# Kernel tuning notes

Measured on AMD Instinct MI355X. Metric: run time of the kernel, lower is better.

Reference implementation:

```python
import jax, jax.numpy as jnp
import numpy as np

MOL_SIZE = 64      # points per molecule (all molecules equal-size -> block-diagonal attn)
NUM_HEADS = 8
CUTOFF = 8.0
NUM_RBF = 32
LN_EPS = 1e-5


def setup_inputs() -> dict:
    key = jax.random.key(0)
    ks = jax.random.split(key, 6)
    B, K, hidden = 1024, MOL_SIZE, 512
    H = NUM_HEADS
    N = B * K
    h = jax.random.normal(ks[0], (N, hidden), jnp.float32)
    pos = jax.random.normal(ks[1], (N, 3), jnp.float32) * 3.0  # spread so dists hit RBF centers
    batch = jnp.repeat(jnp.arange(B, dtype=jnp.int32), K)
    s = lambda fin: 1.0 / np.sqrt(fin)
    centers = jnp.linspace(0.0, CUTOFF, NUM_RBF).astype(jnp.float32)  # RBFEncoder buffer
    w_rbf = jax.random.normal(ks[2], (NUM_RBF, H), jnp.float32) * s(NUM_RBF)
    b_rbf = jnp.zeros((H,), jnp.float32)
    w_qkv = jax.random.normal(ks[3], (hidden, 3 * hidden), jnp.float32) * s(hidden)
    b_qkv = jnp.zeros((3 * hidden,), jnp.float32)
    w_out = jax.random.normal(ks[4], (hidden, hidden), jnp.float32) * s(hidden)
    b_out = jnp.zeros((hidden,), jnp.float32)
    gamma = jnp.ones((hidden,), jnp.float32)
    beta = jnp.zeros((hidden,), jnp.float32)
    return {"h": h, "pos": pos, "batch": batch, "centers": centers,
            "w_rbf": w_rbf, "b_rbf": b_rbf, "w_qkv": w_qkv, "b_qkv": b_qkv,
            "w_out": w_out, "b_out": b_out, "gamma": gamma, "beta": beta}


def reference(h, pos, batch, centers, w_rbf, b_rbf, w_qkv, b_qkv, w_out, b_out, gamma, beta):
    N, hidden = h.shape
    K = MOL_SIZE
    B = N // K
    H = NUM_HEADS
    D = hidden // H
    width = (CUTOFF / NUM_RBF) ** 2
    scale = D ** -0.5

    # equal-size contiguous molecules -> reshape equals per-molecule loop
    hb = h.reshape(B, K, hidden)
    pb = pos.reshape(B, K, 3)

    qkv = hb @ w_qkv + b_qkv                      # [B,K,3*hidden]
    q, k, v = jnp.split(qkv, 3, axis=-1)
    q = q.reshape(B, K, H, D)
    k = k.reshape(B, K, H, D)
    v = v.reshape(B, K, H, D)

    diff = pb[:, :, None, :] - pb[:, None, :, :]  # [B,K,K,3]
    dist = jnp.sqrt(jnp.maximum(jnp.sum(diff * diff, axis=-1), 1e-12))  # torch.cdist
    rbf = jnp.exp(-((dist[..., None] - centers) ** 2) / width)          # [B,K,K,R]
    bias = jnp.transpose(rbf @ w_rbf + b_rbf, (0, 3, 1, 2))             # [B,H,K,K]

    attn = jnp.einsum('bkhd,bjhd->bhkj', q, k) * scale + bias
    attn = jax.nn.softmax(attn, axis=-1)
    agg = jnp.einsum('bhkj,bjhd->bkhd', attn, v).reshape(B, K, hidden)
    out = agg @ w_out + b_out

    y = hb + out
    mu = jnp.mean(y, axis=-1, keepdims=True)
    var = jnp.var(y, axis=-1, keepdims=True)
    y = (y - mu) / jnp.sqrt(var + LN_EPS) * gamma + beta
    return y.reshape(N, hidden)
```

## Files before the change

### kernel.cpp

```cpp
#include <hip/hip_runtime.h>
#include <hip/hip_bf16.h>


#define HID 512
#define TBL 1024
#define DMAX 12.0f

typedef __attribute__((ext_vector_type(4))) float f32x4;
typedef __attribute__((ext_vector_type(8))) short bhalf8;

__device__ __forceinline__ short f2bf(float f) {
    union { float f; unsigned u; } x; x.f = f;
    unsigned u = x.u;
    unsigned r = (u + 0x7FFFu + ((u >> 16) & 1u)) >> 16;
    return (short)r;
}

__device__ __forceinline__ void gld_lds16(const void* g, void* l) {
    __builtin_amdgcn_global_load_lds((const __attribute__((address_space(1))) void*)g,
                                     (__attribute__((address_space(3))) void*)l, 16, 0, 0);
}

__global__ __launch_bounds__(256) void k_prep_w(const float* __restrict__ w_qkv,
                                                const float* __restrict__ w_out,
                                                short* __restrict__ wqT,
                                                short* __restrict__ woT) {
    __shared__ short tile[64][68];
    const int t = threadIdx.x;
    int bt = blockIdx.x;
    const float* src; short* dst; int sld, tk, tc, swz;
    if (bt < 192) { src = w_qkv; dst = wqT; sld = 1536; tk = bt & 7; tc = bt >> 3; swz = 1; }
    else { int b2 = bt - 192; src = w_out; dst = woT; sld = 512; tk = b2 & 7; tc = b2 >> 3; swz = 0; }
#pragma unroll
    for (int p = 0; p < 4; ++p) {
        int s = t + 256 * p;
        int r = s >> 4, sg = s & 15;
        const float4 v = *(const float4*)(src + (tk * 64 + r) * sld + tc * 64 + sg * 4);
        tile[r][sg * 4 + 0] = f2bf(v.x);
        tile[r][sg * 4 + 1] = f2bf(v.y);
        tile[r][sg * 4 + 2] = f2bf(v.z);
        tile[r][sg * 4 + 3] = f2bf(v.w);
    }
    __syncthreads();
#pragma unroll
    for (int p = 0; p < 16; ++p) {
        int o = t + 256 * p;
        int c = o >> 6, k = o & 63;
        int kk = swz ? (k ^ ((c & 7) << 3)) : k;
        dst[(tc * 64 + c) * 512 + tk * 64 + kk] = tile[k][c];
    }
}

__global__ __launch_bounds__(256) void k_prep_tbl(const float* __restrict__ centers,
                                                  const float* __restrict__ w_rbf,
                                                  const float* __restrict__ b_rbf,
                                                  float* __restrict__ tbl) {
    int idx = blockIdx.x * 256 + threadIdx.x;
    int hh = idx >> 10, i = idx & (TBL - 1);
    float d = (float)i * (DMAX / (float)(TBL - 1));
    float s = b_rbf[hh];
    const float invw = 1.0f / 0.0625f;
#pragma unroll 4
    for (int r = 0; r < 32; ++r) {
        float tt = d - centers[r];
        s += w_rbf[r * 8 + hh] * expf(-(tt * tt) * invw);
    }
    tbl[idx] = s;
}

__global__ __launch_bounds__(256) void k_prep_h(const float* __restrict__ h,
                                                short* __restrict__ hbf,
                                                int molbase) {
    size_t i = ((size_t)blockIdx.x * 256 + threadIdx.x) * 8;
    const float* src = h + (size_t)molbase * 64 * HID + i;
    float4 a = *(const float4*)src;
    float4 b = *(const float4*)(src + 4);
    short s8[8];
    s8[0] = f2bf(a.x); s8[1] = f2bf(a.y); s8[2] = f2bf(a.z); s8[3] = f2bf(a.w);
    s8[4] = f2bf(b.x); s8[5] = f2bf(b.y); s8[6] = f2bf(b.z); s8[7] = f2bf(b.w);
    int row = (int)(i >> 9);
    size_t o = i ^ (size_t)((row & 7) << 3);
    *(int4*)(hbf + o) = *(int4*)s8;
}

__global__ __launch_bounds__(512) void k_qkv(const short* __restrict__ hbf,
                                             const float* __restrict__ b_qkv,
                                             const short* __restrict__ wqT,
                                             short* __restrict__ qkvb) {
    __shared__ __align__(16) short As[128 * 64];
    __shared__ __align__(16) short Bs[256 * 64];
    const int t = threadIdx.x;
    const int lane = t & 63, wave = t >> 6;
    const int l16 = lane & 15, g = lane >> 4;
    const int wrow = wave >> 2, wcol = wave & 3;

    int wg = blockIdx.x;
    wg = (wg & 7) * 192 + (wg >> 3);
    const int bx = wg & 255, by = wg >> 8;
    const int R0l = bx * 128;
    const int C0 = by * 256;

    f32x4 acc[4][4];
#pragma unroll
    for (int i = 0; i < 4; ++i)
#pragma unroll
        for (int j = 0; j < 4; ++j) acc[i][j] = (f32x4){0.f, 0.f, 0.f, 0.f};

    const int lrow = lane >> 3, lslot = lane & 7;
    const int axor = (l16 & 7) << 3;

    for (int kc = 0; kc < 8; ++kc) {
        const int kb = kc * 64;
#pragma unroll
        for (int j = 0; j < 2; ++j) {
            int row = wave * 16 + j * 8 + lrow;
            gld_lds16(hbf + (size_t)(R0l + row) * HID + kb + lslot * 8,
                      (char*)As + wave * 2048 + j * 1024 + lane * 16);
        }
#pragma unroll
        for (int j = 0; j < 4; ++j) {
            int row = wave * 32 + j * 8 + lrow;
            gld_lds16(wqT + (size_t)(C0 + row) * HID + kb + lslot * 8,
                      (char*)Bs + wave * 4096 + j * 1024 + lane * 16);
        }
        __syncthreads();
#pragma unroll
        for (int kk = 0; kk < 2; ++kk) {
            const int c8 = kk * 32 + g * 8;
            const int cs = c8 ^ axor;
            bhalf8 af[4], bf[4];
#pragma unroll
            for (int mt = 0; mt < 4; ++mt)
                af[mt] = *(const bhalf8*)(&As[(wrow * 64 + mt * 16 + l16) * 64 + cs]);
#pragma unroll
            for (int nt = 0; nt < 4; ++nt)
                bf[nt] = *(const bhalf8*)(&Bs[(wcol * 64 + nt * 16 + l16) * 64 + cs]);
#pragma unroll
            for (int mt = 0; mt < 4; ++mt)
#pragma unroll
                for (int nt = 0; nt < 4; ++nt)
                    acc[mt][nt] = __builtin_amdgcn_mfma_f32_16x16x32_bf16(
                        af[mt], bf[nt], acc[mt][nt], 0, 0, 0);
        }
        __syncthreads();
    }

    const int sec = C0 >> 9;
    const float mul = (sec == 0) ? 0.125f : 1.0f;
#pragma unroll
    for (int nt = 0; nt < 4; ++nt) {
        int c = C0 + wcol * 64 + nt * 16 + l16;
        float bv = b_qkv[c];
        int head = (c >> 6) & 7, d = c & 63;
#pragma unroll
        for (int mt = 0; mt < 4; ++mt) {
            int rowl = R0l + wrow * 64 + mt * 16 + g * 4;
            int mol_local = rowl >> 6;
            int rloc = rowl & 63;
            short* panel = qkvb + (size_t)((mol_local * 3 + sec) * 8 + head) * 4096;
            if (sec == 2) {
                short4 s4;
                s4.x = f2bf(acc[mt][nt][0] + bv);
                s4.y = f2bf(acc[mt][nt][1] + bv);
                s4.z = f2bf(acc[mt][nt][2] + bv);
                s4.w = f2bf(acc[mt][nt][3] + bv);
                *(short4*)(panel + d * 64 + rloc) = s4;
            } else {
#pragma unroll
                for (int r = 0; r < 4; ++r)
                    panel[(rloc + r) * 64 + d] = f2bf((acc[mt][nt][r] + bv) * mul);
            }
        }
    }
}

__global__ __launch_bounds__(512) void k_fused(const short* __restrict__ qkvb,
                                               const float* __restrict__ pos,
                                               const float* __restrict__ tbl,
                                               const float* __restrict__ h,
                                               const short* __restrict__ woT,
                                               const float* __restrict__ b_out,
                                               const float* __restrict__ gamma,
                                               const float* __restrict__ beta,
                                               float* __restrict__ out,
                                               int molbase) {
    __shared__ __align__(16) short uP[8 * 4096];
    __shared__ float s_tbl[8 * 1032];
    __shared__ float s_px[64], s_py[64], s_pz[64];
    __shared__ float red[64 * 16];
    __shared__ float mr[64 * 2];

    const int t = threadIdx.x;
    const int wave = t >> 6, lane = t & 63;
    const int l16 = lane & 15, g = lane >> 4;
    const int mol_local = blockIdx.x;
    const int rowbase = (molbase + mol_local) * 64;

    for (int i = t; i < 8 * TBL; i += 512)
        s_tbl[(i >> 10) * 1032 + (i & (TBL - 1))] = tbl[i];
    if (t < 64) {
        s_px[t] = pos[(rowbase + t) * 3 + 0];
        s_py[t] = pos[(rowbase + t) * 3 + 1];
        s_pz[t] = pos[(rowbase + t) * 3 + 2];
    }
    __syncthreads();

    const short* qp = qkvb + ((size_t)(mol_local * 3 + 0) * 8 + wave) * 4096;
    const short* kp = qkvb + ((size_t)(mol_local * 3 + 1) * 8 + wave) * 4096;
    const short* vt = qkvb + ((size_t)(mol_local * 3 + 2) * 8 + wave) * 4096;

    f32x4 sacc[4][4];
#pragma unroll
    for (int i = 0; i < 4; ++i)
#pragma unroll
        for (int j = 0; j < 4; ++j) sacc[i][j] = (f32x4){0.f, 0.f, 0.f, 0.f};
#pragma unroll
    for (int kk = 0; kk < 2; ++kk) {
        bhalf8 qa[4], kb[4];
#pragma unroll
        for (int mt = 0; mt < 4; ++mt)
            qa[mt] = *(const bhalf8*)(qp + (mt * 16 + l16) * 64 + kk * 32 + g * 8);
#pragma unroll
        for (int nt = 0; nt < 4; ++nt)
            kb[nt] = *(const bhalf8*)(kp + (nt * 16 + l16) * 64 + kk * 32 + g * 8);
#pragma unroll
        for (int mt = 0; mt < 4; ++mt)
#pragma unroll
            for (int nt = 0; nt < 4; ++nt)
                sacc[mt][nt] = __builtin_amdgcn_mfma_f32_16x16x32_bf16(
                    qa[mt], kb[nt], sacc[mt][nt], 0, 0, 0);
    }

    const float tscale = (float)(TBL - 1) / DMAX;
    const float* T = s_tbl + wave * 1032;
#pragma unroll
    for (int nt = 0; nt < 4; ++nt) {
        int col = nt * 16 + l16;
        float cx = s_px[col], cy = s_py[col], cz = s_pz[col];
#pragma unroll
        for (int mt = 0; mt < 4; ++mt) {
#pragma unroll
            for (int r = 0; r < 4; ++r) {
                int row = mt * 16 + g * 4 + r;
                float dx = s_px[row] - cx, dy = s_py[row] - cy, dz = s_pz[row] - cz;
                float dd = fmaf(dx, dx, fmaf(dy, dy, dz * dz));
                float dist = sqrtf(fmaxf(dd, 1e-12f));
                float u = fminf(dist, DMAX) * tscale;
                int i = (int)u; if (i > TBL - 2) i = TBL - 2;
                float fr = u - (float)i;
                float t0 = T[i];
                sacc[mt][nt][r] += fmaf(fr, T[i + 1] - t0, t0);
            }
        }
    }

    float inv[4][4];
    short* Pw = uP + wave * 4096;
#pragma unroll
    for (int mt = 0; mt < 4; ++mt) {
#pragma unroll
        for (int r = 0; r < 4; ++r) {
            float m = fmaxf(fmaxf(sacc[mt][0][r], sacc[mt][1][r]),
                            fmaxf(sacc[mt][2][r], sacc[mt][3][r]));
#pragma unroll
            for (int off = 1; off < 16; off <<= 1) m = fmaxf(m, __shfl_xor(m, off, 64));
            float e[4], ssum = 0.f;
#pragma unroll
            for (int nt = 0; nt < 4; ++nt) { e[nt] = __expf(sacc[mt][nt][r] - m); ssum += e[nt]; }
#pragma unroll
            for (int off = 1; off < 16; off <<= 1) ssum += __shfl_xor(ssum, off, 64);
            inv[mt][r] = 1.0f / ssum;
            int row = mt * 16 + g * 4 + r;
            int rho = row & 7;
#pragma unroll
            for (int nt = 0; nt < 4; ++nt) {
                int c = nt * 16 + l16;
                Pw[row * 64 + (((c >> 3) ^ rho) << 3) + (c & 7)] = f2bf(e[nt]);
            }
        }
    }

    f32x4 oacc[4][4];
#pragma unroll
    for (int i = 0; i < 4; ++i)
#pragma unroll
        for (int j = 0; j < 4; ++j) oacc[i][j] = (f32x4){0.f, 0.f, 0.f, 0.f};
#pragma unroll
    for (int kk = 0; kk < 2; ++kk) {
        bhalf8 pa[4], vb[4];
#pragma unroll
        for (int mt = 0; mt < 4; ++mt)
            pa[mt] = *(const bhalf8*)(Pw + (mt * 16 + l16) * 64 +
                                      (((kk * 4 + g) ^ (l16 & 7)) << 3));
#pragma unroll
        for (int nt = 0; nt < 4; ++nt)
            vb[nt] = *(const bhalf8*)(vt + (nt * 16 + l16) * 64 + kk * 32 + g * 8);
#pragma unroll
        for (int mt = 0; mt < 4; ++mt)
#pragma unroll
            for (int nt = 0; nt < 4; ++nt)
                oacc[mt][nt] = __builtin_amdgcn_mfma_f32_16x16x32_bf16(
                    pa[mt], vb[nt], oacc[mt][nt], 0, 0, 0);
    }
#pragma unroll
    for (int mt = 0; mt < 4; ++mt)
#pragma unroll
        for (int nt = 0; nt < 4; ++nt)
#pragma unroll
            for (int r = 0; r < 4; ++r) oacc[mt][nt][r] *= inv[mt][r];

    __syncthreads();

#pragma unroll
    for (int mt = 0; mt < 4; ++mt) {
#pragma unroll
        for (int r = 0; r < 4; ++r) {
            int row = mt * 16 + g * 4 + r;
            int rho = row & 7;
#pragma unroll
            for (int nt = 0; nt < 4; ++nt) {
                int c = wave * 64 + nt * 16 + l16;
                uP[row * 512 + (((c >> 3) ^ rho) << 3) + (c & 7)] = f2bf(oacc[mt][nt][r]);
            }
        }
    }
    __syncthreads();

    f32x4 pacc[4][4];
#pragma unroll
    for (int i = 0; i < 4; ++i)
#pragma unroll
        for (int j = 0; j < 4; ++j) pacc[i][j] = (f32x4){0.f, 0.f, 0.f, 0.f};
#pragma unroll 4
    for (int kc = 0; kc < 16; ++kc) {
        bhalf8 af[4], bw[4];
#pragma unroll
        for (int mt = 0; mt < 4; ++mt)
            af[mt] = *(const bhalf8*)(uP + (mt * 16 + l16) * 512 +
                                      (((kc * 4 + g) ^ (l16 & 7)) << 3));
#pragma unroll
        for (int nt = 0; nt < 4; ++nt)
            bw[nt] = *(const bhalf8*)(woT + (size_t)(wave * 64 + nt * 16 + l16) * HID +
                                      kc * 32 + g * 8);
#pragma unroll
        for (int mt = 0; mt < 4; ++mt)
#pragma unroll
            for (int nt = 0; nt < 4; ++nt)
                pacc[mt][nt] = __builtin_amdgcn_mfma_f32_16x16x32_bf16(
                    af[mt], bw[nt], pacc[mt][nt], 0, 0, 0);
    }

#pragma unroll
    for (int mt = 0; mt < 4; ++mt) {
#pragma unroll
        for (int r = 0; r < 4; ++r) {
            int row = mt * 16 + g * 4 + r;
            float rs = 0.f, rq = 0.f;
#pragma unroll
            for (int nt = 0; nt < 4; ++nt) {
                int col = wave * 64 + nt * 16 + l16;
                float v = pacc[mt][nt][r] + b_out[col] +
                          h[(size_t)(rowbase + row) * HID + col];
                pacc[mt][nt][r] = v;
                rs += v;
                rq = fmaf(v, v, rq);
            }
#pragma unroll
            for (int off = 1; off < 16; off <<= 1) {
                rs += __shfl_xor(rs, off, 64);
                rq += __shfl_xor(rq, off, 64);
            }
            if (l16 == 0) {
                red[row * 16 + wave * 2 + 0] = rs;
                red[row * 16 + wave * 2 + 1] = rq;
            }
        }
    }
    __syncthreads();
    if (t < 64) {
        float s = 0.f, q = 0.f;
#pragma unroll
        for (int w = 0; w < 8; ++w) {
            s += red[t * 16 + w * 2 + 0];
            q += red[t * 16 + w * 2 + 1];
        }
        float mean = s * (1.0f / 512.0f);
        float var = q * (1.0f / 512.0f) - mean * mean;
        mr[t * 2 + 0] = mean;
        mr[t * 2 + 1] = rsqrtf(var + 1e-5f);
    }
    __syncthreads();
#pragma unroll
    for (int mt = 0; mt < 4; ++mt) {
#pragma unroll
        for (int r = 0; r < 4; ++r) {
            int row = mt * 16 + g * 4 + r;
            float mean = mr[row * 2 + 0], rstd = mr[row * 2 + 1];
#pragma unroll
            for (int nt = 0; nt < 4; ++nt) {
                int col = wave * 64 + nt * 16 + l16;
                out[(size_t)(rowbase + row) * HID + col] =
                    fmaf((pacc[mt][nt][r] - mean) * rstd, gamma[col], beta[col]);
            }
        }
    }
}

extern "C" void kernel_launch(void* const* d_in, const int* in_sizes, int n_in,
                              void* d_out, int out_size, void* d_ws, size_t ws_size,
                              hipStream_t stream) {
    (void)in_sizes; (void)n_in; (void)out_size; (void)ws_size;
    const float* h       = (const float*)d_in[0];
    const float* pos     = (const float*)d_in[1];
    const float* centers = (const float*)d_in[3];
    const float* w_rbf   = (const float*)d_in[4];
    const float* b_rbf   = (const float*)d_in[5];
    const float* w_qkv   = (const float*)d_in[6];
    const float* b_qkv   = (const float*)d_in[7];
    const float* w_out   = (const float*)d_in[8];
    const float* b_out   = (const float*)d_in[9];
    const float* gamma   = (const float*)d_in[10];
    const float* beta    = (const float*)d_in[11];
    float* out = (float*)d_out;

    char* ws = (char*)d_ws;
    short* wqT  = (short*)ws;
    short* woT  = (short*)(ws + 1572864);
    float* tbl  = (float*)(ws + 2097152);
    short* hbf  = (short*)(ws + 2162688);
    short* qkvb = (short*)(ws + 35717120);

    k_prep_w<<<256, 256, 0, stream>>>(w_qkv, w_out, wqT, woT);
    k_prep_tbl<<<32, 256, 0, stream>>>(centers, w_rbf, b_rbf, tbl);
    for (int half = 0; half < 2; ++half) {
        int molbase = half * 512;
        k_prep_h<<<8192, 256, 0, stream>>>(h, hbf, molbase);
        k_qkv<<<1536, 512, 0, stream>>>(hbf, b_qkv, wqT, qkvb);
        k_fused<<<512, 512, 0, stream>>>(qkvb, pos, tbl, h, woT, b_out,
                                         gamma, beta, out, molbase);
    }
}
```

Baseline: 408.7 us.

## Shrink fused-kernel LDS footprint via chunked P staging and half-row out-projection

```diff
diff --git a/kernel.cpp b/kernel.cpp
--- a/kernel.cpp
+++ b/kernel.cpp
@@ -3,7 +3,7 @@
 
 
 #define HID 512
-#define TBL 1024
+#define TBL 512
 #define DMAX 12.0f
 
 typedef __attribute__((ext_vector_type(4))) float f32x4;
@@ -56,7 +56,7 @@
                                                   const float* __restrict__ b_rbf,
                                                   float* __restrict__ tbl) {
     int idx = blockIdx.x * 256 + threadIdx.x;
-    int hh = idx >> 10, i = idx & (TBL - 1);
+    int hh = idx >> 9, i = idx & (TBL - 1);
     float d = (float)i * (DMAX / (float)(TBL - 1));
     float s = b_rbf[hh];
     const float invw = 1.0f / 0.0625f;
@@ -126,8 +126,7 @@
         __syncthreads();
 #pragma unroll
         for (int kk = 0; kk < 2; ++kk) {
-            const int c8 = kk * 32 + g * 8;
-            const int cs = c8 ^ axor;
+            const int cs = (kk * 32 + g * 8) ^ axor;
             bhalf8 af[4], bf[4];
 #pragma unroll
             for (int mt = 0; mt < 4; ++mt)
@@ -174,30 +173,30 @@
     }
 }
 
-__global__ __launch_bounds__(512) void k_fused(const short* __restrict__ qkvb,
-                                               const float* __restrict__ pos,
-                                               const float* __restrict__ tbl,
-                                               const float* __restrict__ h,
-                                               const short* __restrict__ woT,
-                                               const float* __restrict__ b_out,
-                                               const float* __restrict__ gamma,
-                                               const float* __restrict__ beta,
-                                               float* __restrict__ out,
-                                               int molbase) {
-    __shared__ __align__(16) short uP[8 * 4096];
-    __shared__ float s_tbl[8 * 1032];
+__global__ __launch_bounds__(512, 4) void k_fused(const short* __restrict__ qkvb,
+                                                  const float* __restrict__ pos,
+                                                  const float* __restrict__ tbl,
+                                                  const float* __restrict__ h,
+                                                  const short* __restrict__ woT,
+                                                  const float* __restrict__ b_out,
+                                                  const float* __restrict__ gamma,
+                                                  const float* __restrict__ beta,
+                                                  float* __restrict__ out,
+                                                  int molbase) {
+    __shared__ __align__(16) short uPA[20480];
+    __shared__ float s_tblred[8 * 516];
+    __shared__ float s_dc[64 * 66];
     __shared__ float s_px[64], s_py[64], s_pz[64];
-    __shared__ float red[64 * 16];
-    __shared__ float mr[64 * 2];
 
     const int t = threadIdx.x;
     const int wave = t >> 6, lane = t & 63;
     const int l16 = lane & 15, g = lane >> 4;
     const int mol_local = blockIdx.x;
     const int rowbase = (molbase + mol_local) * 64;
+    const float tscale = (float)(TBL - 1) / DMAX;
 
     for (int i = t; i < 8 * TBL; i += 512)
-        s_tbl[(i >> 10) * 1032 + (i & (TBL - 1))] = tbl[i];
+        s_tblred[(i >> 9) * 516 + (i & (TBL - 1))] = tbl[i];
     if (t < 64) {
         s_px[t] = pos[(rowbase + t) * 3 + 0];
         s_py[t] = pos[(rowbase + t) * 3 + 1];
@@ -205,6 +204,20 @@
     }
     __syncthreads();
 
+    {
+        int row = t >> 3, c0 = (t & 7) * 8;
+        float rx = s_px[row], ry = s_py[row], rz = s_pz[row];
+#pragma unroll
+        for (int j = 0; j < 8; ++j) {
+            int col = c0 + j;
+            float dx = rx - s_px[col], dy = ry - s_py[col], dz = rz - s_pz[col];
+            float dd = fmaf(dx, dx, fmaf(dy, dy, dz * dz));
+            float dist = sqrtf(fmaxf(dd, 1e-12f));
+            s_dc[row * 66 + col] = fminf(dist, DMAX) * tscale;
+        }
+    }
+    __syncthreads();
+
     const short* qp = qkvb + ((size_t)(mol_local * 3 + 0) * 8 + wave) * 4096;
     const short* kp = qkvb + ((size_t)(mol_local * 3 + 1) * 8 + wave) * 4096;
     const short* vt = qkvb + ((size_t)(mol_local * 3 + 2) * 8 + wave) * 4096;
@@ -231,21 +244,16 @@
                     qa[mt], kb[nt], sacc[mt][nt], 0, 0, 0);
     }
 
-    const float tscale = (float)(TBL - 1) / DMAX;
-    const float* T = s_tbl + wave * 1032;
+    const float* T = s_tblred + wave * 516;
 #pragma unroll
     for (int nt = 0; nt < 4; ++nt) {
         int col = nt * 16 + l16;
-        float cx = s_px[col], cy = s_py[col], cz = s_pz[col];
 #pragma unroll
         for (int mt = 0; mt < 4; ++mt) {
 #pragma unroll
             for (int r = 0; r < 4; ++r) {
                 int row = mt * 16 + g * 4 + r;
-                float dx = s_px[row] - cx, dy = s_py[row] - cy, dz = s_pz[row] - cz;
-                float dd = fmaf(dx, dx, fmaf(dy, dy, dz * dz));
-                float dist = sqrtf(fmaxf(dd, 1e-12f));
-                float u = fminf(dist, DMAX) * tscale;
+                float u = s_dc[row * 66 + col];
                 int i = (int)u; if (i > TBL - 2) i = TBL - 2;
                 float fr = u - (float)i;
                 float t0 = T[i];
@@ -254,8 +262,6 @@
         }
     }
 
-    float inv[4][4];
-    short* Pw = uP + wave * 4096;
 #pragma unroll
     for (int mt = 0; mt < 4; ++mt) {
 #pragma unroll
@@ -264,19 +270,18 @@
                             fmaxf(sacc[mt][2][r], sacc[mt][3][r]));
 #pragma unroll
             for (int off = 1; off < 16; off <<= 1) m = fmaxf(m, __shfl_xor(m, off, 64));
-            float e[4], ssum = 0.f;
-#pragma unroll
-            for (int nt = 0; nt < 4; ++nt) { e[nt] = __expf(sacc[mt][nt][r] - m); ssum += e[nt]; }
+            float e0 = __expf(sacc[mt][0][r] - m);
+            float e1 = __expf(sacc[mt][1][r] - m);
+            float e2 = __expf(sacc[mt][2][r] - m);
+            float e3 = __expf(sacc[mt][3][r] - m);
+            float ssum = (e0 + e1) + (e2 + e3);
 #pragma unroll
             for (int off = 1; off < 16; off <<= 1) ssum += __shfl_xor(ssum, off, 64);
-            inv[mt][r] = 1.0f / ssum;
-            int row = mt * 16 + g * 4 + r;
-            int rho = row & 7;
-#pragma unroll
-            for (int nt = 0; nt < 4; ++nt) {
-                int c = nt * 16 + l16;
-                Pw[row * 64 + (((c >> 3) ^ rho) << 3) + (c & 7)] = f2bf(e[nt]);
-            }
+            float inv = 1.0f / ssum;
+            sacc[mt][0][r] = e0 * inv;
+            sacc[mt][1][r] = e1 * inv;
+            sacc[mt][2][r] = e2 * inv;
+            sacc[mt][3][r] = e3 * inv;
         }
     }
 
@@ -285,124 +290,135 @@
     for (int i = 0; i < 4; ++i)
 #pragma unroll
         for (int j = 0; j < 4; ++j) oacc[i][j] = (f32x4){0.f, 0.f, 0.f, 0.f};
-#pragma unroll
-    for (int kk = 0; kk < 2; ++kk) {
+    short* Pw = uPA + wave * 2560;
+#pragma unroll
+    for (int ch = 0; ch < 2; ++ch) {
+        __builtin_amdgcn_sched_barrier(0);
+#pragma unroll
+        for (int mt = 0; mt < 4; ++mt)
+#pragma unroll
+            for (int r = 0; r < 4; ++r) {
+                int row = mt * 16 + g * 4 + r;
+                Pw[row * 40 + l16]      = f2bf(sacc[mt][2 * ch][r]);
+                Pw[row * 40 + 16 + l16] = f2bf(sacc[mt][2 * ch + 1][r]);
+            }
+        __builtin_amdgcn_sched_barrier(0);
         bhalf8 pa[4], vb[4];
 #pragma unroll
         for (int mt = 0; mt < 4; ++mt)
-            pa[mt] = *(const bhalf8*)(Pw + (mt * 16 + l16) * 64 +
-                                      (((kk * 4 + g) ^ (l16 & 7)) << 3));
+            pa[mt] = *(const bhalf8*)(Pw + (mt * 16 + l16) * 40 + g * 8);
 #pragma unroll
         for (int nt = 0; nt < 4; ++nt)
-            vb[nt] = *(const bhalf8*)(vt + (nt * 16 + l16) * 64 + kk * 32 + g * 8);
+            vb[nt] = *(const bhalf8*)(vt + (nt * 16 + l16) * 64 + ch * 32 + g * 8);
 #pragma unroll
         for (int mt = 0; mt < 4; ++mt)
 #pragma unroll
             for (int nt = 0; nt < 4; ++nt)
                 oacc[mt][nt] = __builtin_amdgcn_mfma_f32_16x16x32_bf16(
                     pa[mt], vb[nt], oacc[mt][nt], 0, 0, 0);
-    }
-#pragma unroll
-    for (int mt = 0; mt < 4; ++mt)
-#pragma unroll
-        for (int nt = 0; nt < 4; ++nt)
-#pragma unroll
-            for (int r = 0; r < 4; ++r) oacc[mt][nt][r] *= inv[mt][r];
-
+        __builtin_amdgcn_sched_barrier(0);
+    }
     __syncthreads();
 
-#pragma unroll
-    for (int mt = 0; mt < 4; ++mt) {
-#pragma unroll
-        for (int r = 0; r < 4; ++r) {
-            int row = mt * 16 + g * 4 + r;
-            int rho = row & 7;
-#pragma unroll
-            for (int nt = 0; nt < 4; ++nt) {
-                int c = wave * 64 + nt * 16 + l16;
-                uP[row * 512 + (((c >> 3) ^ rho) << 3) + (c & 7)] = f2bf(oacc[mt][nt][r]);
-            }
-        }
-    }
-    __syncthreads();
-
-    f32x4 pacc[4][4];
-#pragma unroll
-    for (int i = 0; i < 4; ++i)
-#pragma unroll
-        for (int j = 0; j < 4; ++j) pacc[i][j] = (f32x4){0.f, 0.f, 0.f, 0.f};
+    float* redf = s_tblred;
+    float* mrf  = s_tblred + 1024;
+#pragma unroll
+    for (int p = 0; p < 2; ++p) {
+#pragma unroll
+        for (int mt2 = 0; mt2 < 2; ++mt2) {
+            const int mt = p * 2 + mt2;
+#pragma unroll
+            for (int r = 0; r < 4; ++r) {
+                int rl = mt2 * 16 + g * 4 + r;
+                int rho = rl & 7;
+#pragma unroll
+                for (int nt = 0; nt < 4; ++nt) {
+                    int c = wave * 64 + nt * 16 + l16;
+                    uPA[rl * 512 + (((c >> 3) ^ rho) << 3) + (c & 7)] = f2bf(oacc[mt][nt][r]);
+                }
+            }
+        }
+        __syncthreads();
+
+        f32x4 pacc[2][4];
+#pragma unroll
+        for (int i = 0; i < 2; ++i)
+#pragma unroll
+            for (int j = 0; j < 4; ++j) pacc[i][j] = (f32x4){0.f, 0.f, 0.f, 0.f};
 #pragma unroll 4
-    for (int kc = 0; kc < 16; ++kc) {
-        bhalf8 af[4], bw[4];
-#pragma unroll
-        for (int mt = 0; mt < 4; ++mt)
-            af[mt] = *(const bhalf8*)(uP + (mt * 16 + l16) * 512 +
-                                      (((kc * 4 + g) ^ (l16 & 7)) << 3));
-#pragma unroll
-        for (int nt = 0; nt < 4; ++nt)
-            bw[nt] = *(const bhalf8*)(woT + (size_t)(wave * 64 + nt * 16 + l16) * HID +
-                                      kc * 32 + g * 8);
-#pragma unroll
-        for (int mt = 0; mt < 4; ++mt)
+        for (int kc = 0; kc < 16; ++kc) {
+            bhalf8 af[2], bw[4];
+#pragma unroll
+            for (int pt = 0; pt < 2; ++pt) {
+                int rl = pt * 16 + l16;
+                af[pt] = *(const bhalf8*)(uPA + rl * 512 + (((kc * 4 + g) ^ (rl & 7)) << 3));
+            }
 #pragma unroll
             for (int nt = 0; nt < 4; ++nt)
-                pacc[mt][nt] = __builtin_amdgcn_mfma_f32_16x16x32_bf16(
-                    af[mt], bw[nt], pacc[mt][nt], 0, 0, 0);
-    }
-
-#pragma unroll
-    for (int mt = 0; mt < 4; ++mt) {
-#pragma unroll
-        for (int r = 0; r < 4; ++r) {
-            int row = mt * 16 + g * 4 + r;
-            float rs = 0.f, rq = 0.f;
-#pragma unroll
-            for (int nt = 0; nt < 4; ++nt) {
-                int col = wave * 64 + nt * 16 + l16;
-                float v = pacc[mt][nt][r] + b_out[col] +
-                          h[(size_t)(rowbase + row) * HID + col];
-                pacc[mt][nt][r] = v;
-                rs += v;
-                rq = fmaf(v, v, rq);
-            }
-#pragma unroll
-            for (int off = 1; off < 16; off <<= 1) {
-                rs += __shfl_xor(rs, off, 64);
-                rq += __shfl_xor(rq, off, 64);
-            }
-            if (l16 == 0) {
-                red[row * 16 + wave * 2 + 0] = rs;
-                red[row * 16 + wave * 2 + 1] = rq;
-            }
-        }
-    }
-    __syncthreads();
-    if (t < 64) {
-        float s = 0.f, q = 0.f;
-#pragma unroll
-        for (int w = 0; w < 8; ++w) {
-            s += red[t * 16 + w * 2 + 0];
-            q += red[t * 16 + w * 2 + 1];
-        }
-        float mean = s * (1.0f / 512.0f);
-        float var = q * (1.0f / 512.0f) - mean * mean;
-        mr[t * 2 + 0] = mean;
-        mr[t * 2 + 1] = rsqrtf(var + 1e-5f);
-    }
-    __syncthreads();
-#pragma unroll
-    for (int mt = 0; mt < 4; ++mt) {
-#pragma unroll
-        for (int r = 0; r < 4; ++r) {
-            int row = mt * 16 + g * 4 + r;
-            float mean = mr[row * 2 + 0], rstd = mr[row * 2 + 1];
-#pragma unroll
-            for (int nt = 0; nt < 4; ++nt) {
-                int col = wave * 64 + nt * 16 + l16;
-                out[(size_t)(rowbase + row) * HID + col] =
-                    fmaf((pacc[mt][nt][r] - mean) * rstd, gamma[col], beta[col]);
-            }
-        }
+                bw[nt] = *(const bhalf8*)(woT + (size_t)(wave * 64 + nt * 16 + l16) * HID +
+                                          kc * 32 + g * 8);
+#pragma unroll
+            for (int pt = 0; pt < 2; ++pt)
+#pragma unroll
+                for (int nt = 0; nt < 4; ++nt)
+                    pacc[pt][nt] = __builtin_amdgcn_mfma_f32_16x16x32_bf16(
+                        af[pt], bw[nt], pacc[pt][nt], 0, 0, 0);
+        }
+
+#pragma unroll
+        for (int pt = 0; pt < 2; ++pt) {
+#pragma unroll
+            for (int r = 0; r < 4; ++r) {
+                int row = pt * 16 + g * 4 + r;
+                int grow = rowbase + p * 32 + row;
+                float rs = 0.f, rq = 0.f;
+#pragma unroll
+                for (int nt = 0; nt < 4; ++nt) {
+                    int col = wave * 64 + nt * 16 + l16;
+                    float v = pacc[pt][nt][r] + b_out[col] + h[(size_t)grow * HID + col];
+                    pacc[pt][nt][r] = v;
+                    rs += v;
+                    rq = fmaf(v, v, rq);
+                }
+#pragma unroll
+                for (int off = 1; off < 16; off <<= 1) {
+                    rs += __shfl_xor(rs, off, 64);
+                    rq += __shfl_xor(rq, off, 64);
+                }
+                if (l16 == 0) {
+                    redf[(row * 8 + wave) * 2 + 0] = rs;
+                    redf[(row * 8 + wave) * 2 + 1] = rq;
+                }
+            }
+        }
+        __syncthreads();
+        if (t < 32) {
+            float s = 0.f, q = 0.f;
+#pragma unroll
+            for (int w = 0; w < 8; ++w) {
+                s += redf[(t * 8 + w) * 2 + 0];
+                q += redf[(t * 8 + w) * 2 + 1];
+            }
+            float mean = s * (1.0f / 512.0f);
+            float var = q * (1.0f / 512.0f) - mean * mean;
+            mrf[t * 2 + 0] = mean;
+            mrf[t * 2 + 1] = rsqrtf(var + 1e-5f);
+        }
+        __syncthreads();
+#pragma unroll
+        for (int pt = 0; pt < 2; ++pt)
+#pragma unroll
+            for (int r = 0; r < 4; ++r) {
+                int row = pt * 16 + g * 4 + r;
+                int grow = rowbase + p * 32 + row;
+                float mean = mrf[row * 2 + 0], rstd = mrf[row * 2 + 1];
+#pragma unroll
+                for (int nt = 0; nt < 4; ++nt) {
+                    int col = wave * 64 + nt * 16 + l16;
+                    out[(size_t)grow * HID + col] =
+                        fmaf((pacc[pt][nt][r] - mean) * rstd, gamma[col], beta[col]);
+                }
+            }
     }
 }
 
@@ -431,7 +447,7 @@
     short* qkvb = (short*)(ws + 35717120);
 
     k_prep_w<<<256, 256, 0, stream>>>(w_qkv, w_out, wqT, woT);
-    k_prep_tbl<<<32, 256, 0, stream>>>(centers, w_rbf, b_rbf, tbl);
+    k_prep_tbl<<<16, 256, 0, stream>>>(centers, w_rbf, b_rbf, tbl);
     for (int half = 0; half < 2; ++half) {
         int molbase = half * 512;
         k_prep_h<<<8192, 256, 0, stream>>>(h, hbf, molbase);
```

Measured after the change: 496.8 us. +21.5%, slower.
